# Optimization experiments

Hardware: AMD Instinct MI355X
Metric: run time of the kernel (lower is better)

Reference implementation:

```python
import jax, jax.numpy as jnp
import numpy as np

LN_EPS = 1e-5


def setup_inputs() -> dict:
    key = jax.random.key(0)
    k1, k2, k3 = jax.random.split(key, 3)
    B, L, D = 8, 2048, 512
    K, Dc = 8192, 16
    x = jax.random.normal(k1, (B, L, D), dtype=jnp.float32)
    # xavier_uniform for Linear(dim -> codebook_dim), weight shape (Dc, D)
    bound = float(np.sqrt(6.0 / (D + Dc)))
    proj_weight = jax.random.uniform(k2, (Dc, D), dtype=jnp.float32, minval=-bound, maxval=bound)
    codebook = jax.random.normal(k3, (K, Dc), dtype=jnp.float32)
    return {"x": x, "proj_weight": proj_weight, "codebook": codebook}


def reference(x, proj_weight, codebook):
    # random projection: (B,L,D) @ (D,Dc) -> (B,L,Dc)
    h = jnp.einsum("bld,cd->blc", x, proj_weight)
    # LayerNorm over last dim, no affine params
    mu = jnp.mean(h, axis=-1, keepdims=True)
    var = jnp.mean(jnp.square(h - mu), axis=-1, keepdims=True)
    h = (h - mu) / jnp.sqrt(var + LN_EPS)
    # squared-distance via dot-product decomposition; avoids (B,L,K,Dc) blowup.
    # argmin of ||h - c||^2 == argmin of ||h - c|| (sqrt is monotone).
    h2 = jnp.sum(jnp.square(h), axis=-1, keepdims=True)        # (B,L,1)
    c2 = jnp.sum(jnp.square(codebook), axis=-1)                # (K,)
    dots = jnp.einsum("blc,kc->blk", h, codebook)              # (B,L,K)
    dist2 = h2 - 2.0 * dots + c2                               # (B,L,K)
    codes = jnp.argmin(dist2, axis=-1)                         # (B,L) int
    return codes
```

## Files before the change

kernel.cpp:

```cpp
#include <hip/hip_runtime.h>
#include <math.h>

#define LN_EPS 1e-5f

typedef _Float16 f16;
typedef _Float16 f16x8 __attribute__((ext_vector_type(8)));
typedef _Float16 f16x2 __attribute__((ext_vector_type(2)));
typedef float f32x4 __attribute__((ext_vector_type(4)));
typedef unsigned long long ull;

constexpr int DC = 16;
constexpr int K = 8192;
constexpr int NTOK = 16384;
constexpr int KSPLIT = 32;
constexpr int KCHUNK = K / KSPLIT;
constexpr int JT = 8;
constexpr float SCALE = 16384.f;
constexpr int XPITCH = 520;

__global__ __launch_bounds__(256) void prep_proj(const float* __restrict__ x,
                                                 const float* __restrict__ w,
                                                 const float* __restrict__ cb,
                                                 f16* __restrict__ hB,
                                                 f16* __restrict__ cbA,
                                                 float* __restrict__ c2s) {
  const int tid = threadIdx.x;

  if (blockIdx.x >= NTOK / 16) {
    const int ti = tid >> 6;
    const int l = tid & 63;
    const int ct = (blockIdx.x - NTOK / 16) * 4 + ti;
    const int code = ct * 16 + (l & 15);
    const int g = l >> 4;

    const float* row = cb + (size_t)code * DC + (g & 1) * 8;
    f32x4 v0 = *(const f32x4*)row;
    f32x4 v1 = *(const f32x4*)(row + 4);
    float vv[8] = {v0[0], v0[1], v0[2], v0[3], v1[0], v1[1], v1[2], v1[3]};

    f16x8 r;
#pragma unroll
    for (int p = 0; p < 8; ++p) {
      float cc = -128.f * vv[p];
      f16 hh = (f16)cc;
      r[p] = (g < 2) ? hh : (f16)(cc - (float)hh);
    }
    *(f16x8*)(cbA + ((size_t)ct * 64 + l) * 8) = r;

    if (g == 0) {
      const f32x4* rw = (const f32x4*)(cb + (size_t)code * DC);
      f32x4 a0 = rw[0], a1 = rw[1], a2 = rw[2], a3 = rw[3];
      float s = 0.f;
#pragma unroll
      for (int p = 0; p < 4; ++p)
        s += a0[p] * a0[p] + a1[p] * a1[p] + a2[p] * a2[p] + a3[p] * a3[p];
      c2s[code] = (s + 16.5f) * SCALE;
    }
    return;
  }

  __shared__ float xs[16 * XPITCH];
  __shared__ float wsh[16 * 516];
  __shared__ float hsm[16][17];
  const size_t base = (size_t)blockIdx.x * (16 * 512);

  const float4* xg = (const float4*)(x + base);
#pragma unroll
  for (int i = 0; i < 8; ++i) {
    int idx = tid + 256 * i;
    int tok = idx >> 7;
    int d4 = idx & 127;
    *(float4*)&xs[tok * XPITCH + d4 * 4] = xg[idx];
  }

  const float4* wg = (const float4*)w;
#pragma unroll
  for (int i = 0; i < 8; ++i) {
    int idx = tid + 256 * i;
    int c = idx >> 7;
    int d4 = idx & 127;
    *(float4*)&wsh[c * 516 + d4 * 4] = wg[idx];
  }
  __syncthreads();

  const int tok = tid >> 4;
  const int c = tid & 15;
  const float4* xr = (const float4*)(xs + tok * XPITCH);
  const float4* wr = (const float4*)(wsh + c * 516);
  float acc0 = 0.f, acc1 = 0.f, acc2 = 0.f, acc3 = 0.f;
#pragma unroll 16
  for (int d4 = 0; d4 < 128; ++d4) {
    float4 xv = xr[d4];
    float4 wv = wr[d4];
    acc0 = fmaf(xv.x, wv.x, acc0);
    acc1 = fmaf(xv.y, wv.y, acc1);
    acc2 = fmaf(xv.z, wv.z, acc2);
    acc3 = fmaf(xv.w, wv.w, acc3);
  }
  float hv = (acc0 + acc1) + (acc2 + acc3);

  float s = hv;
  s += __shfl_xor(s, 1, 16);
  s += __shfl_xor(s, 2, 16);
  s += __shfl_xor(s, 4, 16);
  s += __shfl_xor(s, 8, 16);
  float mu = s * (1.f / 16.f);
  float diff = hv - mu;
  float v = diff * diff;
  v += __shfl_xor(v, 1, 16);
  v += __shfl_xor(v, 2, 16);
  v += __shfl_xor(v, 4, 16);
  v += __shfl_xor(v, 8, 16);
  float var = v * (1.f / 16.f);
  hsm[tok][c] = diff / sqrtf(var + LN_EPS);
  __syncthreads();

  const int l = tid >> 2;
  const int q = tid & 3;
  const int col = l & 15;
  const int g = l >> 4;
  const int s0 = g * 8 + q * 2;
  f16x2 u;
#pragma unroll
  for (int e = 0; e < 2; ++e) {
    int sE = s0 + e;
    int d = sE & 15;
    float f = hsm[col][d] * 256.f;
    f16 hh = (f16)f;
    u[e] = (sE < 16) ? hh : (f16)(f - (float)hh);
  }
  *(f16x2*)(hB + ((size_t)blockIdx.x * 64 + l) * 8 + q * 2) = u;
}

__global__ __launch_bounds__(256, 4) void argmin_mfma(
    const f16* __restrict__ cbA, const float* __restrict__ c2s,
    const f16* __restrict__ hB, ull* __restrict__ pk) {
  const int tid = threadIdx.x;
  const int w = tid >> 6;
  const int lane = tid & 63;
  const int kt0 = blockIdx.y * (KCHUNK / 16);
  const int tt0 = blockIdx.x * (4 * JT) + w * JT;

  f16x8 b1[JT], b2[JT];
#pragma unroll
  for (int j = 0; j < JT; ++j) {
    const f16* p = hB + ((size_t)(tt0 + j) * 64) * 8;
    b1[j] = *(const f16x8*)&p[lane * 8];
    b2[j] = *(const f16x8*)&p[(lane ^ 32) * 8];
  }

  float best[JT];
  int bidx[JT];
#pragma unroll
  for (int j = 0; j < JT; ++j) {
    best[j] = 3.0e38f;
    bidx[j] = 0;
  }

  const int lkoff = (lane >> 4) * 4;
#pragma unroll 2
  for (int t = 0; t < KCHUNK / 16; ++t) {
    f16x8 a = *(const f16x8*)&cbA[((size_t)(kt0 + t) * 64 + lane) * 8];
    const int kbase = blockIdx.y * KCHUNK + t * 16;
    f32x4 c2v = *(const f32x4*)&c2s[kbase + lkoff];
    const int ib = kbase + lkoff;
#pragma unroll
    for (int j = 0; j < JT; ++j) {
      f32x4 acc =
          __builtin_amdgcn_mfma_f32_16x16x32_f16(a, b1[j], c2v, 0, 0, 0);
      acc = __builtin_amdgcn_mfma_f32_16x16x32_f16(a, b2[j], acc, 0, 0, 0);
#pragma unroll
      for (int r = 0; r < 4; ++r) {
        bool lt = acc[r] < best[j];
        best[j] = lt ? acc[r] : best[j];
        bidx[j] = lt ? (ib + r) : bidx[j];
      }
    }
  }

#pragma unroll
  for (int j = 0; j < JT; ++j) {
    float d = best[j];
    int ix = bidx[j];
#pragma unroll
    for (int off = 16; off <= 32; off <<= 1) {
      float od = __shfl_xor(d, off);
      int oi = __shfl_xor(ix, off);
      bool take = (od < d) || (od == d && oi < ix);
      d = take ? od : d;
      ix = take ? oi : ix;
    }
    d = fmaxf(d, 0.f);
    if (lane < 16) {
      int token = (tt0 + j) * 16 + lane;
      ull key = ((ull)__float_as_uint(d) << 32) | (unsigned)ix;
      pk[(size_t)token * KSPLIT + blockIdx.y] = key;
    }
  }
}

__global__ __launch_bounds__(256) void finalize(const ull* __restrict__ pk,
                                                int* __restrict__ out) {
  int t = blockIdx.x * 256 + threadIdx.x;
  const ull* row = pk + (size_t)t * KSPLIT;
  ull best = row[0];
#pragma unroll
  for (int s = 1; s < KSPLIT; ++s) {
    ull k2 = row[s];
    best = (k2 < best) ? k2 : best;
  }
  out[t] = (int)(unsigned)(best & 0xFFFFFFFFull);
}

extern "C" void kernel_launch(void* const* d_in, const int* in_sizes, int n_in,
                              void* d_out, int out_size, void* d_ws,
                              size_t ws_size, hipStream_t stream) {
  const float* x = (const float*)d_in[0];
  const float* w = (const float*)d_in[1];
  const float* cb = (const float*)d_in[2];

  f16* cbA = (f16*)d_ws;
  float* c2s = (float*)(cbA + (size_t)K * 32);
  f16* hB = (f16*)(c2s + K);
  ull* pk = (ull*)(hB + (size_t)NTOK * 32);

  prep_proj<<<NTOK / 16 + K / 64, 256, 0, stream>>>(x, w, cb, hB, cbA, c2s);
  argmin_mfma<<<dim3(NTOK / (64 * JT), KSPLIT), 256, 0, stream>>>(cbA, c2s,
                                                                  hB, pk);
  finalize<<<NTOK / 256, 256, 0, stream>>>(pk, (int*)d_out);
}
```

Measured before the change: 47.91 us.

## Compute projection with split-f16 MFMA instead of scalar FMA and halve KSPLIT

The scalar fp32 projection x·W in prep_proj is replaced by MFMA 16x16x32 f16 instructions, using a hi/lo f16 split of both x and W to keep near-fp32 accuracy. Each of four waves handles a quarter of the D dimension and the partial results are combined through shared memory. The LayerNorm epsilon is scaled to match the scaled h. KSPLIT drops from 32 to 16, which halves the partial results that finalize has to reduce but gives the argmin kernel fewer, longer blocks. The split-f16 products can shift nearest-code ties slightly compared with the fp32 reference.

```diff
diff --git a/kernel.cpp b/kernel.cpp
--- a/kernel.cpp
+++ b/kernel.cpp
@@ -12,18 +12,17 @@
 constexpr int DC = 16;
 constexpr int K = 8192;
 constexpr int NTOK = 16384;
-constexpr int KSPLIT = 32;
+constexpr int KSPLIT = 16;
 constexpr int KCHUNK = K / KSPLIT;
 constexpr int JT = 8;
 constexpr float SCALE = 16384.f;
-constexpr int XPITCH = 520;
-
-__global__ __launch_bounds__(256) void prep_proj(const float* __restrict__ x,
-                                                 const float* __restrict__ w,
-                                                 const float* __restrict__ cb,
-                                                 f16* __restrict__ hB,
-                                                 f16* __restrict__ cbA,
-                                                 float* __restrict__ c2s) {
+constexpr float EPS_S = LN_EPS * SCALE * SCALE;
+constexpr int XP = 516;
+
+__global__ __launch_bounds__(256, 4) void prep_proj(
+    const float* __restrict__ x, const float* __restrict__ wq,
+    const float* __restrict__ cb, f16* __restrict__ hB,
+    f16* __restrict__ cbA, float* __restrict__ c2s) {
   const int tid = threadIdx.x;
 
   if (blockIdx.x >= NTOK / 16) {
@@ -59,45 +58,73 @@
     return;
   }
 
-  __shared__ float xs[16 * XPITCH];
-  __shared__ float wsh[16 * 516];
+  __shared__ float xs[16 * XP];
+  __shared__ float comb[4 * 16 * 20];
   __shared__ float hsm[16][17];
-  const size_t base = (size_t)blockIdx.x * (16 * 512);
-
-  const float4* xg = (const float4*)(x + base);
+
+  const float4* xg = (const float4*)(x + (size_t)blockIdx.x * (16 * 512));
 #pragma unroll
   for (int i = 0; i < 8; ++i) {
     int idx = tid + 256 * i;
     int tok = idx >> 7;
     int d4 = idx & 127;
-    *(float4*)&xs[tok * XPITCH + d4 * 4] = xg[idx];
-  }
-
-  const float4* wg = (const float4*)w;
-#pragma unroll
-  for (int i = 0; i < 8; ++i) {
-    int idx = tid + 256 * i;
-    int c = idx >> 7;
-    int d4 = idx & 127;
-    *(float4*)&wsh[c * 516 + d4 * 4] = wg[idx];
+    *(float4*)&xs[tok * XP + d4 * 4] = xg[idx];
+  }
+
+  const int w = tid >> 6;
+  const int lane = tid & 63;
+  const int g = lane >> 4;
+  const int c_out = lane & 15;
+  const int doff = (g & 1) * 8;
+  f16x8 aw[8];
+#pragma unroll
+  for (int st = 0; st < 8; ++st) {
+    const int step = w * 8 + st;
+    const float* wp = wq + (size_t)c_out * 512 + step * 16 + doff;
+    f32x4 u0 = *(const f32x4*)wp;
+    f32x4 u1 = *(const f32x4*)(wp + 4);
+    float v[8] = {u0[0], u0[1], u0[2], u0[3], u1[0], u1[1], u1[2], u1[3]};
+    f16x8 r;
+#pragma unroll
+    for (int p = 0; p < 8; ++p) {
+      float f = v[p] * 64.f;
+      f16 h1 = (f16)f;
+      r[p] = (g < 2) ? h1 : (f16)(f - (float)h1);
+    }
+    aw[st] = r;
   }
   __syncthreads();
 
-  const int tok = tid >> 4;
-  const int c = tid & 15;
-  const float4* xr = (const float4*)(xs + tok * XPITCH);
-  const float4* wr = (const float4*)(wsh + c * 516);
-  float acc0 = 0.f, acc1 = 0.f, acc2 = 0.f, acc3 = 0.f;
-#pragma unroll 16
-  for (int d4 = 0; d4 < 128; ++d4) {
-    float4 xv = xr[d4];
-    float4 wv = wr[d4];
-    acc0 = fmaf(xv.x, wv.x, acc0);
-    acc1 = fmaf(xv.y, wv.y, acc1);
-    acc2 = fmaf(xv.z, wv.z, acc2);
-    acc3 = fmaf(xv.w, wv.w, acc3);
-  }
-  float hv = (acc0 + acc1) + (acc2 + acc3);
+  f32x4 acc = {0.f, 0.f, 0.f, 0.f};
+  const int tok = lane & 15;
+#pragma unroll
+  for (int st = 0; st < 8; ++st) {
+    const int step = w * 8 + st;
+    const float* xp = &xs[tok * XP + step * 16 + doff];
+    f32x4 u0 = *(const f32x4*)xp;
+    f32x4 u1 = *(const f32x4*)(xp + 4);
+    float v[8] = {u0[0], u0[1], u0[2], u0[3], u1[0], u1[1], u1[2], u1[3]};
+    f16x8 bh, bl;
+#pragma unroll
+    for (int p = 0; p < 8; ++p) {
+      float f = v[p] * 256.f;
+      f16 h1 = (f16)f;
+      bh[p] = h1;
+      bl[p] = (f16)(f - (float)h1);
+    }
+    f16x8 b1 = (g < 2) ? bh : bl;
+    f16x8 b2 = (g < 2) ? bl : bh;
+    acc = __builtin_amdgcn_mfma_f32_16x16x32_f16(aw[st], b1, acc, 0, 0, 0);
+    acc = __builtin_amdgcn_mfma_f32_16x16x32_f16(aw[st], b2, acc, 0, 0, 0);
+  }
+
+  *(f32x4*)&comb[w * 320 + tok * 20 + g * 4] = acc;
+  __syncthreads();
+
+  const int tokL = tid >> 4;
+  const int cL = tid & 15;
+  float hv = (comb[0 * 320 + tokL * 20 + cL] + comb[1 * 320 + tokL * 20 + cL]) +
+             (comb[2 * 320 + tokL * 20 + cL] + comb[3 * 320 + tokL * 20 + cL]);
 
   float s = hv;
   s += __shfl_xor(s, 1, 16);
@@ -106,20 +133,20 @@
   s += __shfl_xor(s, 8, 16);
   float mu = s * (1.f / 16.f);
   float diff = hv - mu;
-  float v = diff * diff;
-  v += __shfl_xor(v, 1, 16);
-  v += __shfl_xor(v, 2, 16);
-  v += __shfl_xor(v, 4, 16);
-  v += __shfl_xor(v, 8, 16);
-  float var = v * (1.f / 16.f);
-  hsm[tok][c] = diff / sqrtf(var + LN_EPS);
+  float v2 = diff * diff;
+  v2 += __shfl_xor(v2, 1, 16);
+  v2 += __shfl_xor(v2, 2, 16);
+  v2 += __shfl_xor(v2, 4, 16);
+  v2 += __shfl_xor(v2, 8, 16);
+  float var = v2 * (1.f / 16.f);
+  hsm[tokL][cL] = diff / sqrtf(var + EPS_S);
   __syncthreads();
 
-  const int l = tid >> 2;
+  const int le = tid >> 2;
   const int q = tid & 3;
-  const int col = l & 15;
-  const int g = l >> 4;
-  const int s0 = g * 8 + q * 2;
+  const int col = le & 15;
+  const int ge = le >> 4;
+  const int s0 = ge * 8 + q * 2;
   f16x2 u;
 #pragma unroll
   for (int e = 0; e < 2; ++e) {
@@ -129,7 +156,7 @@
     f16 hh = (f16)f;
     u[e] = (sE < 16) ? hh : (f16)(f - (float)hh);
   }
-  *(f16x2*)(hB + ((size_t)blockIdx.x * 64 + l) * 8 + q * 2) = u;
+  *(f16x2*)(hB + ((size_t)blockIdx.x * 64 + le) * 8 + q * 2) = u;
 }
 
 __global__ __launch_bounds__(256, 4) void argmin_mfma(
```

Result: no change. 48.29 us (+0.8%).
